# Performance work log

Hardware: AMD Instinct MI355X
Metric: run time of the kernel (lower is better)

## Reference

```python
import jax, jax.numpy as jnp
import numpy as np

SEQ, D_IN, D_OUT = 4096, 1024, 1024

def setup_inputs() -> dict:
    key = jax.random.key(0)
    k1, k2, k3, k4 = jax.random.split(key, 4)
    return {
        "input": jax.random.normal(k1, (SEQ, D_IN), dtype=jnp.float32),
        "W_query": jax.random.uniform(k2, (D_IN, D_OUT), dtype=jnp.float32),
        "W_key": jax.random.uniform(k3, (D_IN, D_OUT), dtype=jnp.float32),
        "W_value": jax.random.uniform(k4, (D_IN, D_OUT), dtype=jnp.float32),
    }

def reference(input, W_query, W_key, W_value):
    # q, k, v: [S, D_out]
    q = input @ W_query
    k = input @ W_key
    v = input @ W_value
    scale = 1.0 / jnp.sqrt(jnp.asarray(k.shape[-1], dtype=q.dtype))
    scores = (q @ k.T) * scale          # [S, S]
    weights = jax.nn.softmax(scores, axis=-1)
    return weights @ v                  # [S, D_out]
```

## Files before the change

kernel.cpp:

```cpp
#include <hip/hip_runtime.h>
#include <hip/hip_bf16.h>
#include <cstdint>
#include <type_traits>


using u16 = unsigned short;
typedef __attribute__((ext_vector_type(8))) short short8;
typedef __attribute__((ext_vector_type(4))) float floatx4;
typedef __attribute__((ext_vector_type(4))) int intx4;

static constexpr int S_SEQ = 4096;
static constexpr int D_IN  = 1024;
static constexpr int D_OUT = 1024;

__device__ __forceinline__ u16 f2b(float f) {
  uint32_t u = __builtin_bit_cast(uint32_t, f);
  u = (u + 0x7FFFu + ((u >> 16) & 1u)) >> 16;
  return (u16)u;
}
__device__ __forceinline__ float b2f(u16 b) {
  return __builtin_bit_cast(float, (uint32_t)b << 16);
}
__device__ __forceinline__ void load16(const void* g, void* l) {
  __builtin_amdgcn_global_load_lds(
      (const __attribute__((address_space(1))) void*)g,
      (__attribute__((address_space(3))) void*)l,
      16, 0, 0);
}


__global__ void split_bf16_kernel(const float* __restrict__ in,
                                  u16* __restrict__ hi, u16* __restrict__ lo,
                                  int n4) {
  int i = blockIdx.x * blockDim.x + threadIdx.x;
  if (i >= n4) return;
  float4 v = reinterpret_cast<const float4*>(in)[i];
  ushort4 h, l;
  h.x = f2b(v.x); l.x = f2b(v.x - b2f(h.x));
  h.y = f2b(v.y); l.y = f2b(v.y - b2f(h.y));
  h.z = f2b(v.z); l.z = f2b(v.z - b2f(h.z));
  h.w = f2b(v.w); l.w = f2b(v.w - b2f(h.w));
  reinterpret_cast<ushort4*>(hi)[i] = h;
  reinterpret_cast<ushort4*>(lo)[i] = l;
}

__global__ void transpose_w_kernel(const float* __restrict__ Wq,
                                   const float* __restrict__ Wk,
                                   const float* __restrict__ Wv,
                                   u16* __restrict__ WtH, u16* __restrict__ WtL) {
  const int z = blockIdx.z;
  const float* src = (z == 0) ? Wq : (z == 1) ? Wk : Wv;
  u16* dH = WtH + (size_t)z * 1024 * 1024;
  u16* dL = (z < 2) ? WtL + (size_t)z * 1024 * 1024 : nullptr;
  __shared__ float tile[32][33];
  int bx = blockIdx.x * 32, by = blockIdx.y * 32;
  int tx = threadIdx.x, ty = threadIdx.y;
  for (int j = 0; j < 32; j += 8)
    tile[ty + j][tx] = src[(size_t)(by + ty + j) * 1024 + bx + tx];
  __syncthreads();
  for (int j = 0; j < 32; j += 8) {
    float v = tile[tx][ty + j];
    u16 h = f2b(v);
    size_t idx = (size_t)(bx + ty + j) * 1024 + by + tx;
    dH[idx] = h;
    if (dL) dL[idx] = f2b(v - b2f(h));
  }
}

__global__ __launch_bounds__(256)
void qkv_kernel(const u16* __restrict__ Xh, const u16* __restrict__ Xl,
                const u16* __restrict__ WtH, const u16* __restrict__ WtL,
                char* __restrict__ Qa, char* __restrict__ Qb,
                char* __restrict__ Ka, char* __restrict__ Kb,
                u16* __restrict__ Vt) {
  constexpr int BK = 32, K = D_IN;
  constexpr int TILE = 128 * BK;
  __shared__ __align__(16) u16 smem[4 * TILE];
  u16* AsH = smem;
  u16* BsH = smem + TILE;
  u16* AsL = smem + 2 * TILE;
  u16* BsL = smem + 3 * TILE;

  const int tid  = threadIdx.x;
  const int wave = tid >> 6;
  const int lane = tid & 63;
  const int bm   = blockIdx.y * 128;
  const int bn   = blockIdx.x * 128;
  const bool splitB = bn < 2048;
  const int wm   = (wave >> 1) * 64;
  const int wn   = (wave & 1) * 64;
  const int quad = lane >> 4;
  const int l16  = lane & 15;

  const int srow = wave * 16 + (lane >> 2);
  const int scol = (lane & 3) * 8;
  const size_t offA = (size_t)(bm + srow) * K + scol;
  const size_t offB = (size_t)(bn + srow) * K + scol;
  const size_t off64 = (size_t)64 * K;
  const int lds0 = wave * 512;
  const int lds1 = 2048 + wave * 512;

  floatx4 acc[4][4] = {};

  for (int k0 = 0; k0 < K; k0 += BK) {
    __syncthreads();
    load16(Xh + offA + k0,          AsH + lds0);
    load16(Xh + offA + off64 + k0,  AsH + lds1);
    load16(WtH + offB + k0,         BsH + lds0);
    load16(WtH + offB + off64 + k0, BsH + lds1);
    if (splitB) {
      load16(Xl + offA + k0,          AsL + lds0);
      load16(Xl + offA + off64 + k0,  AsL + lds1);
      load16(WtL + offB + k0,         BsL + lds0);
      load16(WtL + offB + off64 + k0, BsL + lds1);
    }
    __syncthreads();

    short8 ah[4], bh[4], al[4], bl[4];
#pragma unroll
    for (int t = 0; t < 4; ++t) {
      ah[t] = *reinterpret_cast<const short8*>(AsH + (wm + t * 16 + l16) * BK + quad * 8);
      bh[t] = *reinterpret_cast<const short8*>(BsH + (wn + t * 16 + l16) * BK + quad * 8);
    }
    if (splitB) {
#pragma unroll
      for (int t = 0; t < 4; ++t) {
        al[t] = *reinterpret_cast<const short8*>(AsL + (wm + t * 16 + l16) * BK + quad * 8);
        bl[t] = *reinterpret_cast<const short8*>(BsL + (wn + t * 16 + l16) * BK + quad * 8);
      }
    }

#pragma unroll
    for (int mt = 0; mt < 4; ++mt)
#pragma unroll
      for (int nt = 0; nt < 4; ++nt)
        acc[mt][nt] = __builtin_amdgcn_mfma_f32_16x16x32_bf16(
            ah[mt], bh[nt], acc[mt][nt], 0, 0, 0);
    if (splitB) {
#pragma unroll
      for (int mt = 0; mt < 4; ++mt)
#pragma unroll
        for (int nt = 0; nt < 4; ++nt) {
          acc[mt][nt] = __builtin_amdgcn_mfma_f32_16x16x32_bf16(
              ah[mt], bl[nt], acc[mt][nt], 0, 0, 0);
          acc[mt][nt] = __builtin_amdgcn_mfma_f32_16x16x32_bf16(
              al[mt], bh[nt], acc[mt][nt], 0, 0, 0);
        }
    }
  }

#pragma unroll
  for (int mt = 0; mt < 4; ++mt) {
#pragma unroll
    for (int nt = 0; nt < 4; ++nt) {
      const int row = bm + wm + mt * 16 + quad * 4;
      const int col = bn + wn + nt * 16 + l16;
      if (bn < 2048) {
        char* Pa = (bn < 1024) ? Qa : Ka;
        char* Pb = (bn < 1024) ? Qb : Kb;
        const int c = (bn < 1024) ? col : col - 1024;
#pragma unroll
        for (int r = 0; r < 4; ++r) {
          float v = acc[mt][nt][r];
          int q16 = (int)rintf(v * 256.f);
          q16 = min(max(q16, -32512), 32512);
          int a = (q16 + 128) >> 8;
          int b = q16 - (a << 8);
          size_t idx = (size_t)(row + r) * 1024 + c;
          Pa[idx] = (char)a;
          Pb[idx] = (char)b;
        }
      } else {
        ushort4 o;
        o.x = f2b(acc[mt][nt][0]);
        o.y = f2b(acc[mt][nt][1]);
        o.z = f2b(acc[mt][nt][2]);
        o.w = f2b(acc[mt][nt][3]);
        *reinterpret_cast<ushort4*>(Vt + (size_t)(col - 2048) * S_SEQ + row) = o;
      }
    }
  }
}

__global__ __launch_bounds__(256)
void s_i8_kernel(const char* __restrict__ Qa, const char* __restrict__ Qb,
                 const char* __restrict__ Ka, const char* __restrict__ Kb,
                 float* __restrict__ S) {
  constexpr int K = D_IN, BK = 128;
  __shared__ __align__(16) char smem[48 * 1024];
  char* QaS = smem;
  char* QbS = smem + 16384;
  char* KaS = smem + 32768;
  char* KbS = smem + 40960;

  const int tid  = threadIdx.x;
  const int wave = tid >> 6;
  const int lane = tid & 63;
  const int bm   = blockIdx.y * 128;
  const int bn   = blockIdx.x * 64;
  const int wm   = (wave >> 1) * 64;
  const int wn   = (wave & 1) * 32;
  const int quad = lane >> 4;
  const int l16  = lane & 15;

  const int srow = lane >> 3;
  const int scol = ((lane & 7) ^ srow) * 16;
  int gQ[4], gK[2];
#pragma unroll
  for (int j = 0; j < 4; ++j)
    gQ[j] = (bm + j * 32 + wave * 8 + srow) * K + scol;
#pragma unroll
  for (int j = 0; j < 2; ++j)
    gK[j] = (bn + j * 32 + wave * 8 + srow) * K + scol;
  const int lQ[4] = {(0 * 32 + wave * 8) * 128, (1 * 32 + wave * 8) * 128,
                     (2 * 32 + wave * 8) * 128, (3 * 32 + wave * 8) * 128};
  const int lK[2] = {(0 * 32 + wave * 8) * 128, (1 * 32 + wave * 8) * 128};

  const int r7 = l16 & 7;
  int cA[4], cB[2];
#pragma unroll
  for (int t = 0; t < 4; ++t)
    cA[t] = (wm + t * 16 + l16) * 128 + ((quad ^ r7) * 16);
#pragma unroll
  for (int t = 0; t < 2; ++t)
    cB[t] = (wn + t * 16 + l16) * 128 + ((quad ^ r7) * 16);

  intx4 accH[4][2] = {};
  intx4 accM[4][2] = {};
  intx4 accL[4][2] = {};

  for (int k0 = 0; k0 < K; k0 += BK) {
    __syncthreads();
#pragma unroll
    for (int j = 0; j < 4; ++j) {
      load16(Qa + gQ[j] + k0, QaS + lQ[j]);
      load16(Qb + gQ[j] + k0, QbS + lQ[j]);
    }
#pragma unroll
    for (int j = 0; j < 2; ++j) {
      load16(Ka + gK[j] + k0, KaS + lK[j]);
      load16(Kb + gK[j] + k0, KbS + lK[j]);
    }
    __syncthreads();

#pragma unroll
    for (int s = 0; s < 2; ++s) {
      const int so = s * 64;
      intx4 ah[4], al[4];
#pragma unroll
      for (int t = 0; t < 4; ++t) {
        ah[t] = *reinterpret_cast<const intx4*>(QaS + (cA[t] ^ so));
        al[t] = *reinterpret_cast<const intx4*>(QbS + (cA[t] ^ so));
      }
#pragma unroll
      for (int nt = 0; nt < 2; ++nt) {
        intx4 bh = *reinterpret_cast<const intx4*>(KaS + (cB[nt] ^ so));
#pragma unroll
        for (int mt = 0; mt < 4; ++mt) {
          accH[mt][nt] = __builtin_amdgcn_mfma_i32_16x16x64_i8(ah[mt], bh, accH[mt][nt], 0, 0, 0);
          accM[mt][nt] = __builtin_amdgcn_mfma_i32_16x16x64_i8(al[mt], bh, accM[mt][nt], 0, 0, 0);
        }
        intx4 bl = *reinterpret_cast<const intx4*>(KbS + (cB[nt] ^ so));
#pragma unroll
        for (int mt = 0; mt < 4; ++mt) {
          accM[mt][nt] = __builtin_amdgcn_mfma_i32_16x16x64_i8(ah[mt], bl, accM[mt][nt], 0, 0, 0);
          accL[mt][nt] = __builtin_amdgcn_mfma_i32_16x16x64_i8(al[mt], bl, accL[mt][nt], 0, 0, 0);
        }
      }
    }
  }

  constexpr float SC = 4.76837158203125e-07f;
#pragma unroll
  for (int mt = 0; mt < 4; ++mt)
#pragma unroll
    for (int nt = 0; nt < 2; ++nt) {
      const int row = bm + wm + mt * 16 + quad * 4;
      const int col = bn + wn + nt * 16 + l16;
#pragma unroll
      for (int r = 0; r < 4; ++r) {
        long long fix = (((long long)accH[mt][nt][r]) << 16) +
                        (((long long)accM[mt][nt][r]) << 8) +
                        (long long)accL[mt][nt][r];
        S[(size_t)(row + r) * S_SEQ + col] = (float)fix * SC;
      }
    }
}

__global__ __launch_bounds__(256)
void pv_kernel(const u16* __restrict__ P, const u16* __restrict__ Vt,
               float* __restrict__ O) {
  constexpr int LDA = S_SEQ;
  constexpr int KS  = S_SEQ / 4;
  constexpr int BK  = 64;
  __shared__ __align__(16) u16 smem[2 * 128 * 64];
  u16* As = smem;
  u16* Bs = smem + 128 * 64;

  const int tid  = threadIdx.x;
  const int wave = tid >> 6;
  const int lane = tid & 63;
  const int bm   = blockIdx.x * 128;
  const int bn   = blockIdx.y * 128;
  const int kz   = blockIdx.z * KS;
  const int wm   = (wave >> 1) * 64;
  const int wn   = (wave & 1) * 64;
  const int quad = lane >> 4;
  const int l16  = lane & 15;

  const int srow  = lane >> 3;
  const int selem = ((lane & 7) ^ srow) * 8;
  size_t gA[4], gB[4];
#pragma unroll
  for (int j = 0; j < 4; ++j) {
    gA[j] = (size_t)(bm + j * 32 + wave * 8 + srow) * LDA + kz + selem;
    gB[j] = (size_t)(bn + j * 32 + wave * 8 + srow) * LDA + kz + selem;
  }
  const int lds[4] = {(wave * 8 + 0) * 64, (wave * 8 + 32) * 64,
                      (wave * 8 + 64) * 64, (wave * 8 + 96) * 64};

  int cA[4], cB[4];
#pragma unroll
  for (int t = 0; t < 4; ++t) {
    const int Ra = wm + t * 16 + l16;
    const int Rb = wn + t * 16 + l16;
    cA[t] = Ra * 64 + ((quad ^ (Ra & 7)) * 8);
    cB[t] = Rb * 64 + ((quad ^ (Rb & 7)) * 8);
  }

  floatx4 acc[4][4] = {};

  for (int k0 = 0; k0 < KS; k0 += BK) {
    __syncthreads();
#pragma unroll
    for (int j = 0; j < 4; ++j) {
      load16(P + gA[j] + k0,  As + lds[j]);
      load16(Vt + gB[j] + k0, Bs + lds[j]);
    }
    __syncthreads();

#pragma unroll
    for (int s = 0; s < 2; ++s) {
      const int so = s * 32;
      short8 af[4], bf[4];
#pragma unroll
      for (int t = 0; t < 4; ++t) {
        af[t] = *reinterpret_cast<const short8*>(As + (cA[t] ^ so));
        bf[t] = *reinterpret_cast<const short8*>(Bs + (cB[t] ^ so));
      }
#pragma unroll
      for (int mt = 0; mt < 4; ++mt)
#pragma unroll
        for (int nt = 0; nt < 4; ++nt)
          acc[mt][nt] = __builtin_amdgcn_mfma_f32_16x16x32_bf16(
              af[mt], bf[nt], acc[mt][nt], 0, 0, 0);
    }
  }

#pragma unroll
  for (int mt = 0; mt < 4; ++mt)
#pragma unroll
    for (int nt = 0; nt < 4; ++nt) {
      const int row = bm + wm + mt * 16 + quad * 4;
      const int col = bn + wn + nt * 16 + l16;
#pragma unroll
      for (int r = 0; r < 4; ++r)
        atomicAdd(&O[(size_t)(row + r) * D_OUT + col], acc[mt][nt][r]);
    }
}

__global__ __launch_bounds__(256)
void softmax_kernel(const float* __restrict__ S, u16* __restrict__ P) {
  const int row = blockIdx.x, tid = threadIdx.x;
  const int lane = tid & 63, wave = tid >> 6;
  __shared__ float red[4];
  const float4* src = reinterpret_cast<const float4*>(S + (size_t)row * S_SEQ);
  ushort4* dst = reinterpret_cast<ushort4*>(P + (size_t)row * S_SEQ);

  float4 v[4];
  float m = -INFINITY;
#pragma unroll
  for (int t = 0; t < 4; ++t) {
    v[t] = src[tid + t * 256];
    m = fmaxf(m, fmaxf(fmaxf(v[t].x, v[t].y), fmaxf(v[t].z, v[t].w)));
  }
#pragma unroll
  for (int off = 1; off < 64; off <<= 1) m = fmaxf(m, __shfl_xor(m, off));
  if (lane == 0) red[wave] = m;
  __syncthreads();
  m = fmaxf(fmaxf(red[0], red[1]), fmaxf(red[2], red[3]));

  float e[16];
  float l = 0.f;
#pragma unroll
  for (int t = 0; t < 4; ++t) {
    e[4 * t + 0] = __expf(v[t].x - m);
    e[4 * t + 1] = __expf(v[t].y - m);
    e[4 * t + 2] = __expf(v[t].z - m);
    e[4 * t + 3] = __expf(v[t].w - m);
    l += e[4 * t + 0] + e[4 * t + 1] + e[4 * t + 2] + e[4 * t + 3];
  }
#pragma unroll
  for (int off = 1; off < 64; off <<= 1) l += __shfl_xor(l, off);
  __syncthreads();
  if (lane == 0) red[wave] = l;
  __syncthreads();
  const float li = 1.f / (red[0] + red[1] + red[2] + red[3]);

#pragma unroll
  for (int t = 0; t < 4; ++t) {
    ushort4 o;
    o.x = f2b(e[4 * t + 0] * li);
    o.y = f2b(e[4 * t + 1] * li);
    o.z = f2b(e[4 * t + 2] * li);
    o.w = f2b(e[4 * t + 3] * li);
    dst[tid + t * 256] = o;
  }
}


extern "C" void kernel_launch(void* const* d_in, const int* in_sizes, int n_in,
                              void* d_out, int out_size, void* d_ws, size_t ws_size,
                              hipStream_t stream) {
  const float* X  = (const float*)d_in[0];
  const float* Wq = (const float*)d_in[1];
  const float* Wk = (const float*)d_in[2];
  const float* Wv = (const float*)d_in[3];
  float* O = (float*)d_out;
  char* ws = (char*)d_ws;

  const size_t MB = 1u << 20;
  u16*   Xh  = (u16*)(ws);
  u16*   Xl  = (u16*)(ws + 8 * MB);
  u16*   WtH = (u16*)(ws + 16 * MB);
  u16*   WtL = (u16*)(ws + 22 * MB);
  u16*   P   = (u16*)(ws);
  char*  Qa  = (char*)(ws + 32 * MB);
  char*  Qb  = (char*)(ws + 36 * MB);
  char*  Ka  = (char*)(ws + 40 * MB);
  char*  Kb  = (char*)(ws + 44 * MB);
  u16*   Vt  = (u16*)(ws + 64 * MB);
  float* Ss  = (float*)(ws + 72 * MB);

  hipMemsetAsync(O, 0, (size_t)S_SEQ * D_OUT * sizeof(float), stream);

  split_bf16_kernel<<<(S_SEQ * D_IN / 4 + 255) / 256, 256, 0, stream>>>(
      X, Xh, Xl, S_SEQ * D_IN / 4);
  transpose_w_kernel<<<dim3(32, 32, 3), dim3(32, 8), 0, stream>>>(
      Wq, Wk, Wv, WtH, WtL);

  qkv_kernel<<<dim3(3072 / 128, S_SEQ / 128), 256, 0, stream>>>(
      Xh, Xl, WtH, WtL, Qa, Qb, Ka, Kb, Vt);

  s_i8_kernel<<<dim3(S_SEQ / 64, S_SEQ / 128), 256, 0, stream>>>(
      Qa, Qb, Ka, Kb, Ss);

  softmax_kernel<<<S_SEQ, 256, 0, stream>>>(Ss, P);

  pv_kernel<<<dim3(S_SEQ / 128, D_OUT / 128, 4), 256, 0, stream>>>(P, Vt, O);
}
```

Measured before the change: 309.5 us.

## Fuse input conversion kernels and replace split-K atomics with bf16 partials plus reduce

The X split and weight transpose kernels are merged into one launch, using a z-slice for X and early exit for surplus x blocks. The memset and fp32 atomicAdd split-K reduction in pv_kernel are replaced by bf16 partial outputs per K-slice, which a new add4 kernel sums into O. The PV grid is reordered so that blockIdx.x walks the output columns, which changes which blocks share rows of P in cache. Storing partials in bf16 costs precision, and the partials reuse the score buffer region.

```diff
diff --git a/kernel.cpp b/kernel.cpp
--- a/kernel.cpp
+++ b/kernel.cpp
@@ -28,33 +28,33 @@
       16, 0, 0);
 }
 
-
-__global__ void split_bf16_kernel(const float* __restrict__ in,
-                                  u16* __restrict__ hi, u16* __restrict__ lo,
-                                  int n4) {
-  int i = blockIdx.x * blockDim.x + threadIdx.x;
-  if (i >= n4) return;
-  float4 v = reinterpret_cast<const float4*>(in)[i];
-  ushort4 h, l;
-  h.x = f2b(v.x); l.x = f2b(v.x - b2f(h.x));
-  h.y = f2b(v.y); l.y = f2b(v.y - b2f(h.y));
-  h.z = f2b(v.z); l.z = f2b(v.z - b2f(h.z));
-  h.w = f2b(v.w); l.w = f2b(v.w - b2f(h.w));
-  reinterpret_cast<ushort4*>(hi)[i] = h;
-  reinterpret_cast<ushort4*>(lo)[i] = l;
-}
-
-__global__ void transpose_w_kernel(const float* __restrict__ Wq,
-                                   const float* __restrict__ Wk,
-                                   const float* __restrict__ Wv,
-                                   u16* __restrict__ WtH, u16* __restrict__ WtL) {
+__global__ void convert_kernel(const float* __restrict__ X,
+                               const float* __restrict__ Wq,
+                               const float* __restrict__ Wk,
+                               const float* __restrict__ Wv,
+                               u16* __restrict__ Xh, u16* __restrict__ Xl,
+                               u16* __restrict__ WtH, u16* __restrict__ WtL) {
   const int z = blockIdx.z;
+  const int tx = threadIdx.x, ty = threadIdx.y;
+  if (z == 3) {
+    const int bid = blockIdx.y * 128 + blockIdx.x;
+    const int i = bid * 256 + ty * 32 + tx;
+    float4 v = reinterpret_cast<const float4*>(X)[i];
+    ushort4 h, l;
+    h.x = f2b(v.x); l.x = f2b(v.x - b2f(h.x));
+    h.y = f2b(v.y); l.y = f2b(v.y - b2f(h.y));
+    h.z = f2b(v.z); l.z = f2b(v.z - b2f(h.z));
+    h.w = f2b(v.w); l.w = f2b(v.w - b2f(h.w));
+    reinterpret_cast<ushort4*>(Xh)[i] = h;
+    reinterpret_cast<ushort4*>(Xl)[i] = l;
+    return;
+  }
+  if (blockIdx.x >= 32) return;
   const float* src = (z == 0) ? Wq : (z == 1) ? Wk : Wv;
   u16* dH = WtH + (size_t)z * 1024 * 1024;
   u16* dL = (z < 2) ? WtL + (size_t)z * 1024 * 1024 : nullptr;
   __shared__ float tile[32][33];
   int bx = blockIdx.x * 32, by = blockIdx.y * 32;
-  int tx = threadIdx.x, ty = threadIdx.y;
   for (int j = 0; j < 32; j += 8)
     tile[ty + j][tx] = src[(size_t)(by + ty + j) * 1024 + bx + tx];
   __syncthreads();
@@ -289,7 +289,7 @@
 
 __global__ __launch_bounds__(256)
 void pv_kernel(const u16* __restrict__ P, const u16* __restrict__ Vt,
-               float* __restrict__ O) {
+               u16* __restrict__ Osl) {
   constexpr int LDA = S_SEQ;
   constexpr int KS  = S_SEQ / 4;
   constexpr int BK  = 64;
@@ -300,8 +300,8 @@
   const int tid  = threadIdx.x;
   const int wave = tid >> 6;
   const int lane = tid & 63;
-  const int bm   = blockIdx.x * 128;
-  const int bn   = blockIdx.y * 128;
+  const int bn   = blockIdx.x * 128;
+  const int bm   = blockIdx.y * 128;
   const int kz   = blockIdx.z * KS;
   const int wm   = (wave >> 1) * 64;
   const int wn   = (wave & 1) * 64;
@@ -357,6 +357,7 @@
     }
   }
 
+  u16* C = Osl + (size_t)blockIdx.z * S_SEQ * D_OUT;
 #pragma unroll
   for (int mt = 0; mt < 4; ++mt)
 #pragma unroll
@@ -365,8 +366,24 @@
       const int col = bn + wn + nt * 16 + l16;
 #pragma unroll
       for (int r = 0; r < 4; ++r)
-        atomicAdd(&O[(size_t)(row + r) * D_OUT + col], acc[mt][nt][r]);
-    }
+        C[(size_t)(row + r) * D_OUT + col] = f2b(acc[mt][nt][r]);
+    }
+}
+
+__global__ void add4_kernel(const u16* __restrict__ s,
+                            float* __restrict__ o, int n4) {
+  int i = blockIdx.x * blockDim.x + threadIdx.x;
+  if (i >= n4) return;
+  ushort4 a = reinterpret_cast<const ushort4*>(s)[i];
+  ushort4 b = reinterpret_cast<const ushort4*>(s)[i + n4];
+  ushort4 c = reinterpret_cast<const ushort4*>(s)[i + 2 * n4];
+  ushort4 d = reinterpret_cast<const ushort4*>(s)[i + 3 * n4];
+  float4 x;
+  x.x = (b2f(a.x) + b2f(b.x)) + (b2f(c.x) + b2f(d.x));
+  x.y = (b2f(a.y) + b2f(b.y)) + (b2f(c.y) + b2f(d.y));
+  x.z = (b2f(a.z) + b2f(b.z)) + (b2f(c.z) + b2f(d.z));
+  x.w = (b2f(a.w) + b2f(b.w)) + (b2f(c.w) + b2f(d.w));
+  reinterpret_cast<float4*>(o)[i] = x;
 }
 
 __global__ __launch_bounds__(256)
@@ -441,13 +458,10 @@
   char*  Kb  = (char*)(ws + 44 * MB);
   u16*   Vt  = (u16*)(ws + 64 * MB);
   float* Ss  = (float*)(ws + 72 * MB);
-
-  hipMemsetAsync(O, 0, (size_t)S_SEQ * D_OUT * sizeof(float), stream);
-
-  split_bf16_kernel<<<(S_SEQ * D_IN / 4 + 255) / 256, 256, 0, stream>>>(
-      X, Xh, Xl, S_SEQ * D_IN / 4);
-  transpose_w_kernel<<<dim3(32, 32, 3), dim3(32, 8), 0, stream>>>(
-      Wq, Wk, Wv, WtH, WtL);
+  u16*   Osl = (u16*)(ws + 72 * MB);
+
+  convert_kernel<<<dim3(128, 32, 4), dim3(32, 8), 0, stream>>>(
+      X, Wq, Wk, Wv, Xh, Xl, WtH, WtL);
 
   qkv_kernel<<<dim3(3072 / 128, S_SEQ / 128), 256, 0, stream>>>(
       Xh, Xl, WtH, WtL, Qa, Qb, Ka, Kb, Vt);
@@ -457,5 +471,7 @@
 
   softmax_kernel<<<S_SEQ, 256, 0, stream>>>(Ss, P);
 
-  pv_kernel<<<dim3(S_SEQ / 128, D_OUT / 128, 4), 256, 0, stream>>>(P, Vt, O);
-}
+  pv_kernel<<<dim3(D_OUT / 128, S_SEQ / 128, 4), 256, 0, stream>>>(P, Vt, Osl);
+  add4_kernel<<<(S_SEQ * D_OUT / 4 + 255) / 256, 256, 0, stream>>>(
+      Osl, O, S_SEQ * D_OUT / 4);
+}
```

Result: faster. 276.8 us (-10.6%).
